# Performance work log

Hardware: AMD Instinct MI355X
Metric: run time of the kernel (lower is better)

The kernel has to match this reference:

```python
import jax, jax.numpy as jnp
import numpy as np

BETA = 0.25
K = 1024  # num_embeddings


def setup_inputs() -> dict:
    key = jax.random.key(0)
    k1, k2 = jax.random.split(key)
    x = jax.random.normal(k1, (32, 64, 64, 64), dtype=jnp.float32)  # [B, D, H, W]
    # nn.Embedding init: uniform(-1/K, 1/K)
    codebook = jax.random.uniform(k2, (K, 64), dtype=jnp.float32,
                                  minval=-1.0 / K, maxval=1.0 / K)
    return {"x": x, "codebook": codebook}


def reference(x, codebook):
    B, D, H, W = x.shape
    xp = jnp.transpose(x, (0, 2, 3, 1))            # [B, H, W, D]
    xf = xp.reshape(-1, D)                          # [N, D]
    # squared euclidean distances; argmin is identical to argmin of cdist
    d2 = (jnp.sum(xf * xf, axis=1, keepdims=True)
          - 2.0 * (xf @ codebook.T)
          + jnp.sum(codebook * codebook, axis=1))   # [N, K]
    idx = jnp.argmin(d2, axis=1)                    # [N]
    x_q = codebook[idx].reshape(xp.shape)           # [B, H, W, D]
    # training loss: codebook term + beta * commitment term
    loss = (jnp.mean((jax.lax.stop_gradient(x_q) - xp) ** 2)
            + BETA * jnp.mean((x_q - jax.lax.stop_gradient(xp)) ** 2))
    # straight-through estimator
    x_st = xp + jax.lax.stop_gradient(x_q - xp)
    out = jnp.transpose(x_st, (0, 3, 1, 2))         # [B, D, H, W]
    return out, loss
```

## Files before the change

kernel.cpp:

```cpp
#include <hip/hip_runtime.h>
#include <cfloat>


#define DD   64
#define HHWW 4096
#define KC   1024
#define NBLK  2048
#define NPOSD 8388608.0f

typedef __bf16  bf16x8 __attribute__((ext_vector_type(8)));
typedef float   f32x4  __attribute__((ext_vector_type(4)));

__device__ __forceinline__ unsigned short bf16_bits(float f) {
  unsigned u = __float_as_uint(f);
  return (unsigned short)((u + 0x7FFFu + ((u >> 16) & 1u)) >> 16);
}

__device__ __forceinline__ unsigned int umax2(unsigned int a, unsigned int b) {
  return a > b ? a : b;
}

__device__ __forceinline__ void gload_lds16(const void* gsrc, void* ldst) {
  __builtin_amdgcn_global_load_lds(
      (const __attribute__((address_space(1))) unsigned int*)gsrc,
      (__attribute__((address_space(3))) unsigned int*)ldst, 16, 0, 0);
}

__global__ __launch_bounds__(256) void vq_pre(
    const float* __restrict__ cb,
    unsigned short* __restrict__ cb_frag,
    float* __restrict__ hneg4)
{
  int k = blockIdx.x * 256 + threadIdx.x;
  if (k >= KC) return;
  float c[DD];
  float sum = 0.f;
#pragma unroll
  for (int d = 0; d < DD; ++d) { c[d] = cb[k * DD + d]; sum += c[d] * c[d]; }
  const float m = 1.0f - 0.5f * sum;
  hneg4[k * 4 + 0] = m; hneg4[k * 4 + 1] = m;
  hneg4[k * 4 + 2] = m; hneg4[k * 4 + 3] = m;
  int t = k >> 4, l15 = k & 15;
#pragma unroll
  for (int kk = 0; kk < 2; ++kk)
#pragma unroll
    for (int g = 0; g < 4; ++g)
#pragma unroll
      for (int e = 0; e < 8; ++e)
        cb_frag[(((t * 2 + kk) * 64) + (g * 16 + l15)) * 8 + e] =
            bf16_bits(c[kk * 32 + g * 8 + e]);
}

__global__ __launch_bounds__(256) void vq_main(
    const float* __restrict__ x,
    const unsigned short* __restrict__ cb_frag,
    const float* __restrict__ hneg4,
    const float* __restrict__ cb,
    float* __restrict__ out,
    float* __restrict__ partials)
{
  __shared__ unsigned short xfrag[4096];
  __shared__ f32x4          mh4_lds[KC];
  __shared__ unsigned int   cand[4][64];
  __shared__ int            idx_lds[64];
  __shared__ float          xred[4];

  const int tid  = threadIdx.x;
  const int wv   = tid >> 6;
  const int lane = tid & 63;
  const int l15  = lane & 15;

  const int row = blockIdx.x;
  const int b   = row >> 6;
  const int h   = row & 63;
  const float* xb = x + (size_t)b * DD * HHWW + h * 64;

#pragma unroll
  for (int i = 0; i < 4; ++i)
    gload_lds16((const char*)hneg4 + i * 4096 + (size_t)tid * 16,
                (char*)mh4_lds + i * 4096 + wv * 1024);

  float xacc = 0.f;
#pragma unroll
  for (int r4 = 0; r4 < 4; ++r4) {
    const int m  = tid + r4 * 256;
    const int d  = m >> 4;
    const int w4 = m & 15;
    const float4 v4 = *(const float4*)(xb + (size_t)d * HHWW + w4 * 4);
    const int kk = d >> 5, gg = (d >> 3) & 3, e = d & 7;
    const int pt = w4 >> 2;
    const int base = pt * 1024 + kk * 512 + gg * 128 + e;
    const int lb = (w4 & 3) * 4;
    xacc += v4.x * v4.x + v4.y * v4.y + v4.z * v4.z + v4.w * v4.w;
    xfrag[base + (lb + 0) * 8] = bf16_bits(v4.x);
    xfrag[base + (lb + 1) * 8] = bf16_bits(v4.y);
    xfrag[base + (lb + 2) * 8] = bf16_bits(v4.z);
    xfrag[base + (lb + 3) * 8] = bf16_bits(v4.w);
  }

  __syncthreads();

  bf16x8 afrag[4][2];
#pragma unroll
  for (int pt = 0; pt < 4; ++pt) {
    afrag[pt][0] = *(const bf16x8*)(&xfrag[pt * 1024 + lane * 8]);
    afrag[pt][1] = *(const bf16x8*)(&xfrag[pt * 1024 + 512 + lane * 8]);
  }

  unsigned int best[4][4];
#pragma unroll
  for (int pt = 0; pt < 4; ++pt)
#pragma unroll
    for (int rr = 0; rr < 4; ++rr) best[pt][rr] = 0u;

  const unsigned int MASK = 0xFFFFFC00u;
  const int codec0 = 1023 - wv * 256 - l15;
  const char*  bb  = (const char*)cb_frag + (size_t)wv * 16 * 2048 + (size_t)lane * 16;
  const f32x4* mhp = mh4_lds + wv * 256 + l15;

  bf16x8 nb0 = *(const bf16x8*)(bb);
  bf16x8 nb1 = *(const bf16x8*)(bb + 1024);
  f32x4  nmh = mhp[0];

#pragma unroll 4
  for (int t = 0; t < 16; ++t) {
    const bf16x8 b0 = nb0, b1 = nb1;
    const f32x4  mh = nmh;
    const char* bn = bb + (size_t)(((t + 1) & 15) * 2048);
    nb0 = *(const bf16x8*)(bn);
    nb1 = *(const bf16x8*)(bn + 1024);
    nmh = mhp[((t + 1) & 15) * 16];

    const unsigned int codec = (unsigned int)(codec0 - t * 16);

    f32x4 acc[4];
#pragma unroll
    for (int pt = 0; pt < 4; ++pt)
      acc[pt] = __builtin_amdgcn_mfma_f32_16x16x32_bf16(afrag[pt][0], b0, mh, 0, 0, 0);
#pragma unroll
    for (int pt = 0; pt < 4; ++pt)
      acc[pt] = __builtin_amdgcn_mfma_f32_16x16x32_bf16(afrag[pt][1], b1, acc[pt], 0, 0, 0);

#pragma unroll
    for (int pt = 0; pt < 4; ++pt)
#pragma unroll
      for (int rr = 0; rr < 4; ++rr) {
        const unsigned int p = (__float_as_uint(acc[pt][rr]) & MASK) | codec;
        best[pt][rr] = umax2(best[pt][rr], p);
      }
  }

  const int g = lane >> 4;
#pragma unroll
  for (int pt = 0; pt < 4; ++pt)
#pragma unroll
    for (int rr = 0; rr < 4; ++rr) {
      unsigned int v = best[pt][rr];
#pragma unroll
      for (int m = 1; m < 16; m <<= 1) {
        unsigned int vo = __shfl_xor(v, m, 64);
        v = umax2(v, vo);
      }
      if (l15 == 0) cand[wv][pt * 16 + g * 4 + rr] = v;
    }

#pragma unroll
  for (int m = 1; m < 64; m <<= 1) xacc += __shfl_xor(xacc, m, 64);
  if (lane == 0) xred[wv] = xacc;

  __syncthreads();

  if (tid < 64) {
    unsigned int v01 = umax2(cand[0][tid], cand[1][tid]);
    unsigned int v23 = umax2(cand[2][tid], cand[3][tid]);
    unsigned int v   = umax2(v01, v23);
    idx_lds[tid] = 1023 - (int)(v & 1023u);
    float vt1 = __uint_as_float(v & MASK) - 1.0f;
#pragma unroll
    for (int m = 1; m < 64; m <<= 1) vt1 += __shfl_xor(vt1, m, 64);
    if (tid == 0)
      partials[blockIdx.x] =
          (xred[0] + xred[1] + xred[2] + xred[3]) - 2.0f * vt1;
  }

  __syncthreads();

  const int myidx = idx_lds[lane];
  const float4* crow = (const float4*)(cb + (size_t)myidx * DD) + wv * 4;
  const float4 c0 = crow[0], c1 = crow[1], c2 = crow[2], c3 = crow[3];
  float* ob = out + (size_t)b * DD * HHWW + h * 64 + lane;
  ob[(size_t)(wv * 16 +  0) * HHWW] = c0.x;
  ob[(size_t)(wv * 16 +  1) * HHWW] = c0.y;
  ob[(size_t)(wv * 16 +  2) * HHWW] = c0.z;
  ob[(size_t)(wv * 16 +  3) * HHWW] = c0.w;
  ob[(size_t)(wv * 16 +  4) * HHWW] = c1.x;
  ob[(size_t)(wv * 16 +  5) * HHWW] = c1.y;
  ob[(size_t)(wv * 16 +  6) * HHWW] = c1.z;
  ob[(size_t)(wv * 16 +  7) * HHWW] = c1.w;
  ob[(size_t)(wv * 16 +  8) * HHWW] = c2.x;
  ob[(size_t)(wv * 16 +  9) * HHWW] = c2.y;
  ob[(size_t)(wv * 16 + 10) * HHWW] = c2.z;
  ob[(size_t)(wv * 16 + 11) * HHWW] = c2.w;
  ob[(size_t)(wv * 16 + 12) * HHWW] = c3.x;
  ob[(size_t)(wv * 16 + 13) * HHWW] = c3.y;
  ob[(size_t)(wv * 16 + 14) * HHWW] = c3.z;
  ob[(size_t)(wv * 16 + 15) * HHWW] = c3.w;
}

__global__ __launch_bounds__(256) void vq_loss(
    const float* __restrict__ partials, float* __restrict__ loss_out)
{
  __shared__ float sred[4];
  int tid = threadIdx.x;
  float s = 0.f;
  for (int i = tid; i < NBLK; i += 256) s += partials[i];
#pragma unroll
  for (int m = 1; m < 64; m <<= 1) s += __shfl_xor(s, m, 64);
  if ((tid & 63) == 0) sred[tid >> 6] = s;
  __syncthreads();
  if (tid == 0)
    loss_out[0] = (sred[0] + sred[1] + sred[2] + sred[3]) * (1.25f / NPOSD);
}

extern "C" void kernel_launch(void* const* d_in, const int* in_sizes, int n_in,
                              void* d_out, int out_size, void* d_ws, size_t ws_size,
                              hipStream_t stream) {
  const float* x  = (const float*)d_in[0];
  const float* cb = (const float*)d_in[1];
  float* out      = (float*)d_out;
  float* loss_out = out + 8388608;

  char* ws = (char*)d_ws;
  unsigned short* cb_frag = (unsigned short*)(ws);
  float* hneg4    = (float*)(ws + 131072);
  float* partials = (float*)(ws + 147456);

  vq_pre <<<4,    256, 0, stream>>>(cb, cb_frag, hneg4);
  vq_main<<<NBLK, 256, 0, stream>>>(x, cb_frag, hneg4, cb, out, partials);
  vq_loss<<<1,    256, 0, stream>>>(partials, loss_out);
}
```

Baseline: 45.02 us.

## Process two rows per block, split codebook across wave pairs, drop LDS bias staging

Each block now handles two image rows (128 positions) instead of one, halving the grid to 1024 blocks. The four waves are split into two codebook halves times two position pairs, so each wave walks 512 codes over 32 iterations and reuses every codebook fragment load across four position tiles from two rows. The per-code bias is now read straight from global memory instead of being staged into LDS with global_load_lds, and the final argmin merges two candidates instead of four. The aim is to amortise codebook fragment traffic over more positions and cut LDS setup. The cost is fewer blocks on the machine and a longer serial loop per wave.

```diff
diff --git a/kernel.cpp b/kernel.cpp
--- a/kernel.cpp
+++ b/kernel.cpp
@@ -2,10 +2,10 @@
 #include <cfloat>
 
 
-#define DD   64
-#define HHWW 4096
-#define KC   1024
-#define NBLK  2048
+#define DD    64
+#define HHWW  4096
+#define KC    1024
+#define NBLKM 1024
 #define NPOSD 8388608.0f
 
 typedef __bf16  bf16x8 __attribute__((ext_vector_type(8)));
@@ -18,12 +18,6 @@
 
 __device__ __forceinline__ unsigned int umax2(unsigned int a, unsigned int b) {
   return a > b ? a : b;
-}
-
-__device__ __forceinline__ void gload_lds16(const void* gsrc, void* ldst) {
-  __builtin_amdgcn_global_load_lds(
-      (const __attribute__((address_space(1))) unsigned int*)gsrc,
-      (__attribute__((address_space(3))) unsigned int*)ldst, 16, 0, 0);
 }
 
 __global__ __launch_bounds__(256) void vq_pre(
@@ -59,110 +53,114 @@
     float* __restrict__ out,
     float* __restrict__ partials)
 {
-  __shared__ unsigned short xfrag[4096];
-  __shared__ f32x4          mh4_lds[KC];
-  __shared__ unsigned int   cand[4][64];
-  __shared__ int            idx_lds[64];
+  __shared__ unsigned short xfrag[2][4096];
+  __shared__ unsigned int   cand[2][2][64];
+  __shared__ int            idx_lds[2][64];
   __shared__ float          xred[4];
+  __shared__ float          vtred[2];
 
   const int tid  = threadIdx.x;
   const int wv   = tid >> 6;
   const int lane = tid & 63;
   const int l15  = lane & 15;
-
-  const int row = blockIdx.x;
-  const int b   = row >> 6;
-  const int h   = row & 63;
-  const float* xb = x + (size_t)b * DD * HHWW + h * 64;
-
-#pragma unroll
-  for (int i = 0; i < 4; ++i)
-    gload_lds16((const char*)hneg4 + i * 4096 + (size_t)tid * 16,
-                (char*)mh4_lds + i * 4096 + wv * 1024);
+  const int g    = lane >> 4;
+  const int cw   = wv & 1;
+  const int pw   = wv >> 1;
+
+  const int row0 = blockIdx.x * 2;
+  const int b    = row0 >> 6;
+  const int h0   = row0 & 63;
+  const float* xb = x + (size_t)b * DD * HHWW + h0 * 64;
 
   float xacc = 0.f;
 #pragma unroll
-  for (int r4 = 0; r4 < 4; ++r4) {
-    const int m  = tid + r4 * 256;
-    const int d  = m >> 4;
-    const int w4 = m & 15;
-    const float4 v4 = *(const float4*)(xb + (size_t)d * HHWW + w4 * 4);
-    const int kk = d >> 5, gg = (d >> 3) & 3, e = d & 7;
-    const int pt = w4 >> 2;
-    const int base = pt * 1024 + kk * 512 + gg * 128 + e;
-    const int lb = (w4 & 3) * 4;
-    xacc += v4.x * v4.x + v4.y * v4.y + v4.z * v4.z + v4.w * v4.w;
-    xfrag[base + (lb + 0) * 8] = bf16_bits(v4.x);
-    xfrag[base + (lb + 1) * 8] = bf16_bits(v4.y);
-    xfrag[base + (lb + 2) * 8] = bf16_bits(v4.z);
-    xfrag[base + (lb + 3) * 8] = bf16_bits(v4.w);
-  }
-
-  __syncthreads();
-
-  bf16x8 afrag[4][2];
-#pragma unroll
-  for (int pt = 0; pt < 4; ++pt) {
-    afrag[pt][0] = *(const bf16x8*)(&xfrag[pt * 1024 + lane * 8]);
-    afrag[pt][1] = *(const bf16x8*)(&xfrag[pt * 1024 + 512 + lane * 8]);
-  }
-
-  unsigned int best[4][4];
-#pragma unroll
-  for (int pt = 0; pt < 4; ++pt)
-#pragma unroll
-    for (int rr = 0; rr < 4; ++rr) best[pt][rr] = 0u;
+  for (int r = 0; r < 2; ++r) {
+#pragma unroll
+    for (int r4 = 0; r4 < 4; ++r4) {
+      const int m  = tid + r4 * 256;
+      const int d  = m >> 4;
+      const int w4 = m & 15;
+      const float4 v4 = *(const float4*)(xb + (size_t)d * HHWW + r * 64 + w4 * 4);
+      const int kk = d >> 5, gg = (d >> 3) & 3, e = d & 7;
+      const int pt = w4 >> 2;
+      const int base = pt * 1024 + kk * 512 + gg * 128 + e;
+      const int lb = (w4 & 3) * 4;
+      xacc += v4.x * v4.x + v4.y * v4.y + v4.z * v4.z + v4.w * v4.w;
+      xfrag[r][base + (lb + 0) * 8] = bf16_bits(v4.x);
+      xfrag[r][base + (lb + 1) * 8] = bf16_bits(v4.y);
+      xfrag[r][base + (lb + 2) * 8] = bf16_bits(v4.z);
+      xfrag[r][base + (lb + 3) * 8] = bf16_bits(v4.w);
+    }
+  }
+
+  __syncthreads();
+
+  bf16x8 afrag[2][2][2];
+#pragma unroll
+  for (int r = 0; r < 2; ++r)
+#pragma unroll
+    for (int j = 0; j < 2; ++j) {
+      const int pt = pw * 2 + j;
+      afrag[r][j][0] = *(const bf16x8*)(&xfrag[r][pt * 1024 + lane * 8]);
+      afrag[r][j][1] = *(const bf16x8*)(&xfrag[r][pt * 1024 + 512 + lane * 8]);
+    }
+
+  unsigned int best[2][2][4];
+#pragma unroll
+  for (int r = 0; r < 2; ++r)
+#pragma unroll
+    for (int j = 0; j < 2; ++j)
+#pragma unroll
+      for (int rr = 0; rr < 4; ++rr) best[r][j][rr] = 0u;
 
   const unsigned int MASK = 0xFFFFFC00u;
-  const int codec0 = 1023 - wv * 256 - l15;
-  const char*  bb  = (const char*)cb_frag + (size_t)wv * 16 * 2048 + (size_t)lane * 16;
-  const f32x4* mhp = mh4_lds + wv * 256 + l15;
+  const int codec0 = 1023 - cw * 512 - l15;
+  const char*  bb  = (const char*)cb_frag + (size_t)cw * 32 * 2048 + (size_t)lane * 16;
+  const f32x4* mhp = (const f32x4*)hneg4 + cw * 512 + l15;
 
   bf16x8 nb0 = *(const bf16x8*)(bb);
   bf16x8 nb1 = *(const bf16x8*)(bb + 1024);
   f32x4  nmh = mhp[0];
 
 #pragma unroll 4
-  for (int t = 0; t < 16; ++t) {
+  for (int t = 0; t < 32; ++t) {
     const bf16x8 b0 = nb0, b1 = nb1;
     const f32x4  mh = nmh;
-    const char* bn = bb + (size_t)(((t + 1) & 15) * 2048);
-    nb0 = *(const bf16x8*)(bn);
-    nb1 = *(const bf16x8*)(bn + 1024);
-    nmh = mhp[((t + 1) & 15) * 16];
+    const int tn = (t + 1) & 31;
+    nb0 = *(const bf16x8*)(bb + tn * 2048);
+    nb1 = *(const bf16x8*)(bb + tn * 2048 + 1024);
+    nmh = mhp[tn * 16];
 
     const unsigned int codec = (unsigned int)(codec0 - t * 16);
 
-    f32x4 acc[4];
-#pragma unroll
-    for (int pt = 0; pt < 4; ++pt)
-      acc[pt] = __builtin_amdgcn_mfma_f32_16x16x32_bf16(afrag[pt][0], b0, mh, 0, 0, 0);
-#pragma unroll
-    for (int pt = 0; pt < 4; ++pt)
-      acc[pt] = __builtin_amdgcn_mfma_f32_16x16x32_bf16(afrag[pt][1], b1, acc[pt], 0, 0, 0);
-
-#pragma unroll
-    for (int pt = 0; pt < 4; ++pt)
+#pragma unroll
+    for (int r = 0; r < 2; ++r)
+#pragma unroll
+      for (int j = 0; j < 2; ++j) {
+        f32x4 acc = __builtin_amdgcn_mfma_f32_16x16x32_bf16(afrag[r][j][0], b0, mh, 0, 0, 0);
+        acc = __builtin_amdgcn_mfma_f32_16x16x32_bf16(afrag[r][j][1], b1, acc, 0, 0, 0);
+#pragma unroll
+        for (int rr = 0; rr < 4; ++rr) {
+          const unsigned int p = (__float_as_uint(acc[rr]) & MASK) | codec;
+          best[r][j][rr] = umax2(best[r][j][rr], p);
+        }
+      }
+  }
+
+#pragma unroll
+  for (int r = 0; r < 2; ++r)
+#pragma unroll
+    for (int j = 0; j < 2; ++j)
 #pragma unroll
       for (int rr = 0; rr < 4; ++rr) {
-        const unsigned int p = (__float_as_uint(acc[pt][rr]) & MASK) | codec;
-        best[pt][rr] = umax2(best[pt][rr], p);
+        unsigned int v = best[r][j][rr];
+#pragma unroll
+        for (int m = 1; m < 16; m <<= 1) {
+          unsigned int vo = __shfl_xor(v, m, 64);
+          v = umax2(v, vo);
+        }
+        if (l15 == 0) cand[cw][r][(pw * 2 + j) * 16 + g * 4 + rr] = v;
       }
-  }
-
-  const int g = lane >> 4;
-#pragma unroll
-  for (int pt = 0; pt < 4; ++pt)
-#pragma unroll
-    for (int rr = 0; rr < 4; ++rr) {
-      unsigned int v = best[pt][rr];
-#pragma unroll
-      for (int m = 1; m < 16; m <<= 1) {
-        unsigned int vo = __shfl_xor(v, m, 64);
-        v = umax2(v, vo);
-      }
-      if (l15 == 0) cand[wv][pt * 16 + g * 4 + rr] = v;
-    }
 
 #pragma unroll
   for (int m = 1; m < 64; m <<= 1) xacc += __shfl_xor(xacc, m, 64);
@@ -170,41 +168,45 @@
 
   __syncthreads();
 
-  if (tid < 64) {
-    unsigned int v01 = umax2(cand[0][tid], cand[1][tid]);
-    unsigned int v23 = umax2(cand[2][tid], cand[3][tid]);
-    unsigned int v   = umax2(v01, v23);
-    idx_lds[tid] = 1023 - (int)(v & 1023u);
+  if (tid < 128) {
+    const int r = tid >> 6, p = tid & 63;
+    const unsigned int v = umax2(cand[0][r][p], cand[1][r][p]);
+    idx_lds[r][p] = 1023 - (int)(v & 1023u);
     float vt1 = __uint_as_float(v & MASK) - 1.0f;
 #pragma unroll
     for (int m = 1; m < 64; m <<= 1) vt1 += __shfl_xor(vt1, m, 64);
-    if (tid == 0)
-      partials[blockIdx.x] =
-          (xred[0] + xred[1] + xred[2] + xred[3]) - 2.0f * vt1;
-  }
-
-  __syncthreads();
-
-  const int myidx = idx_lds[lane];
-  const float4* crow = (const float4*)(cb + (size_t)myidx * DD) + wv * 4;
-  const float4 c0 = crow[0], c1 = crow[1], c2 = crow[2], c3 = crow[3];
-  float* ob = out + (size_t)b * DD * HHWW + h * 64 + lane;
-  ob[(size_t)(wv * 16 +  0) * HHWW] = c0.x;
-  ob[(size_t)(wv * 16 +  1) * HHWW] = c0.y;
-  ob[(size_t)(wv * 16 +  2) * HHWW] = c0.z;
-  ob[(size_t)(wv * 16 +  3) * HHWW] = c0.w;
-  ob[(size_t)(wv * 16 +  4) * HHWW] = c1.x;
-  ob[(size_t)(wv * 16 +  5) * HHWW] = c1.y;
-  ob[(size_t)(wv * 16 +  6) * HHWW] = c1.z;
-  ob[(size_t)(wv * 16 +  7) * HHWW] = c1.w;
-  ob[(size_t)(wv * 16 +  8) * HHWW] = c2.x;
-  ob[(size_t)(wv * 16 +  9) * HHWW] = c2.y;
-  ob[(size_t)(wv * 16 + 10) * HHWW] = c2.z;
-  ob[(size_t)(wv * 16 + 11) * HHWW] = c2.w;
-  ob[(size_t)(wv * 16 + 12) * HHWW] = c3.x;
-  ob[(size_t)(wv * 16 + 13) * HHWW] = c3.y;
-  ob[(size_t)(wv * 16 + 14) * HHWW] = c3.z;
-  ob[(size_t)(wv * 16 + 15) * HHWW] = c3.w;
+    if ((tid & 63) == 0) vtred[r] = vt1;
+  }
+
+  __syncthreads();
+
+  if (tid == 0)
+    partials[blockIdx.x] =
+        (xred[0] + xred[1] + xred[2] + xred[3]) - 2.0f * (vtred[0] + vtred[1]);
+
+#pragma unroll
+  for (int r = 0; r < 2; ++r) {
+    const int myidx = idx_lds[r][lane];
+    const float4* crow = (const float4*)(cb + (size_t)myidx * DD) + wv * 4;
+    const float4 c0 = crow[0], c1 = crow[1], c2 = crow[2], c3 = crow[3];
+    float* ob = out + (size_t)b * DD * HHWW + (h0 + r) * 64 + lane;
+    ob[(size_t)(wv * 16 +  0) * HHWW] = c0.x;
+    ob[(size_t)(wv * 16 +  1) * HHWW] = c0.y;
+    ob[(size_t)(wv * 16 +  2) * HHWW] = c0.z;
+    ob[(size_t)(wv * 16 +  3) * HHWW] = c0.w;
+    ob[(size_t)(wv * 16 +  4) * HHWW] = c1.x;
+    ob[(size_t)(wv * 16 +  5) * HHWW] = c1.y;
+    ob[(size_t)(wv * 16 +  6) * HHWW] = c1.z;
+    ob[(size_t)(wv * 16 +  7) * HHWW] = c1.w;
+    ob[(size_t)(wv * 16 +  8) * HHWW] = c2.x;
+    ob[(size_t)(wv * 16 +  9) * HHWW] = c2.y;
+    ob[(size_t)(wv * 16 + 10) * HHWW] = c2.z;
+    ob[(size_t)(wv * 16 + 11) * HHWW] = c2.w;
+    ob[(size_t)(wv * 16 + 12) * HHWW] = c3.x;
+    ob[(size_t)(wv * 16 + 13) * HHWW] = c3.y;
+    ob[(size_t)(wv * 16 + 14) * HHWW] = c3.z;
+    ob[(size_t)(wv * 16 + 15) * HHWW] = c3.w;
+  }
 }
 
 __global__ __launch_bounds__(256) void vq_loss(
@@ -213,7 +215,7 @@
   __shared__ float sred[4];
   int tid = threadIdx.x;
   float s = 0.f;
-  for (int i = tid; i < NBLK; i += 256) s += partials[i];
+  for (int i = tid; i < NBLKM; i += 256) s += partials[i];
 #pragma unroll
   for (int m = 1; m < 64; m <<= 1) s += __shfl_xor(s, m, 64);
   if ((tid & 63) == 0) sred[tid >> 6] = s;
@@ -235,7 +237,7 @@
   float* hneg4    = (float*)(ws + 131072);
   float* partials = (float*)(ws + 147456);
 
-  vq_pre <<<4,    256, 0, stream>>>(cb, cb_frag, hneg4);
-  vq_main<<<NBLK, 256, 0, stream>>>(x, cb_frag, hneg4, cb, out, partials);
-  vq_loss<<<1,    256, 0, stream>>>(partials, loss_out);
-}
+  vq_pre <<<4,     256, 0, stream>>>(cb, cb_frag, hneg4);
+  vq_main<<<NBLKM, 256, 0, stream>>>(x, cb_frag, hneg4, cb, out, partials);
+  vq_loss<<<1,     256, 0, stream>>>(partials, loss_out);
+}
```

Measured after the change: 60.72 us. 1.35x slower.

## Read codebook norms from global instead of LDS and XOR-swizzle x fragments

Applied to the files above, without the earlier changes.

Drops the async global-to-LDS staging of the per-code norm bias array and has each wave read its bias vectors straight from global/L2 inside the MFMA loop. This frees 16 KB of LDS per block, which may allow more resident blocks. It also XOR-swizzles the bf16 x-fragment layout in LDS by pixel tile to cut bank conflicts on the scattered stores. The cost is extra global loads in the inner loop, which now depend on cache hits.

```diff
diff --git a/kernel.cpp b/kernel.cpp
--- a/kernel.cpp
+++ b/kernel.cpp
@@ -18,12 +18,6 @@
 
 __device__ __forceinline__ unsigned int umax2(unsigned int a, unsigned int b) {
   return a > b ? a : b;
-}
-
-__device__ __forceinline__ void gload_lds16(const void* gsrc, void* ldst) {
-  __builtin_amdgcn_global_load_lds(
-      (const __attribute__((address_space(1))) unsigned int*)gsrc,
-      (__attribute__((address_space(3))) unsigned int*)ldst, 16, 0, 0);
 }
 
 __global__ __launch_bounds__(256) void vq_pre(
@@ -60,7 +54,6 @@
     float* __restrict__ partials)
 {
   __shared__ unsigned short xfrag[4096];
-  __shared__ f32x4          mh4_lds[KC];
   __shared__ unsigned int   cand[4][64];
   __shared__ int            idx_lds[64];
   __shared__ float          xred[4];
@@ -74,11 +67,6 @@
   const int b   = row >> 6;
   const int h   = row & 63;
   const float* xb = x + (size_t)b * DD * HHWW + h * 64;
-
-#pragma unroll
-  for (int i = 0; i < 4; ++i)
-    gload_lds16((const char*)hneg4 + i * 4096 + (size_t)tid * 16,
-                (char*)mh4_lds + i * 4096 + wv * 1024);
 
   float xacc = 0.f;
 #pragma unroll
@@ -92,19 +80,21 @@
     const int base = pt * 1024 + kk * 512 + gg * 128 + e;
     const int lb = (w4 & 3) * 4;
     xacc += v4.x * v4.x + v4.y * v4.y + v4.z * v4.z + v4.w * v4.w;
-    xfrag[base + (lb + 0) * 8] = bf16_bits(v4.x);
-    xfrag[base + (lb + 1) * 8] = bf16_bits(v4.y);
-    xfrag[base + (lb + 2) * 8] = bf16_bits(v4.z);
-    xfrag[base + (lb + 3) * 8] = bf16_bits(v4.w);
-  }
-
-  __syncthreads();
-
+    xfrag[base + ((lb + 0) ^ pt) * 8] = bf16_bits(v4.x);
+    xfrag[base + ((lb + 1) ^ pt) * 8] = bf16_bits(v4.y);
+    xfrag[base + ((lb + 2) ^ pt) * 8] = bf16_bits(v4.z);
+    xfrag[base + ((lb + 3) ^ pt) * 8] = bf16_bits(v4.w);
+  }
+
+  __syncthreads();
+
+  const int g = lane >> 4;
   bf16x8 afrag[4][2];
 #pragma unroll
   for (int pt = 0; pt < 4; ++pt) {
-    afrag[pt][0] = *(const bf16x8*)(&xfrag[pt * 1024 + lane * 8]);
-    afrag[pt][1] = *(const bf16x8*)(&xfrag[pt * 1024 + 512 + lane * 8]);
+    const int ls = g * 16 + (l15 ^ pt);
+    afrag[pt][0] = *(const bf16x8*)(&xfrag[pt * 1024 + ls * 8]);
+    afrag[pt][1] = *(const bf16x8*)(&xfrag[pt * 1024 + 512 + ls * 8]);
   }
 
   unsigned int best[4][4];
@@ -116,7 +106,7 @@
   const unsigned int MASK = 0xFFFFFC00u;
   const int codec0 = 1023 - wv * 256 - l15;
   const char*  bb  = (const char*)cb_frag + (size_t)wv * 16 * 2048 + (size_t)lane * 16;
-  const f32x4* mhp = mh4_lds + wv * 256 + l15;
+  const f32x4* mhp = (const f32x4*)hneg4 + wv * 256 + l15;
 
   bf16x8 nb0 = *(const bf16x8*)(bb);
   bf16x8 nb1 = *(const bf16x8*)(bb + 1024);
@@ -126,10 +116,10 @@
   for (int t = 0; t < 16; ++t) {
     const bf16x8 b0 = nb0, b1 = nb1;
     const f32x4  mh = nmh;
-    const char* bn = bb + (size_t)(((t + 1) & 15) * 2048);
-    nb0 = *(const bf16x8*)(bn);
-    nb1 = *(const bf16x8*)(bn + 1024);
-    nmh = mhp[((t + 1) & 15) * 16];
+    const int tn = (t + 1) & 15;
+    nb0 = *(const bf16x8*)(bb + tn * 2048);
+    nb1 = *(const bf16x8*)(bb + tn * 2048 + 1024);
+    nmh = mhp[tn * 16];
 
     const unsigned int codec = (unsigned int)(codec0 - t * 16);
 
@@ -150,7 +140,6 @@
       }
   }
 
-  const int g = lane >> 4;
 #pragma unroll
   for (int pt = 0; pt < 4; ++pt)
 #pragma unroll
```

Result: slower. 46.75 us (+3.8%).
